# Performance work log

Measured on AMD Instinct MI355X. Metric: run time of the kernel, lower is better.

The kernel has to match this reference:

```python
import jax, jax.numpy as jnp
import numpy as np

STRIDE = 1
PADDING = 1
DILATION = 1

def setup_inputs() -> dict:
    key = jax.random.key(0)
    k1, k2, k3 = jax.random.split(key, 3)
    N, C_IN, H, W = 32, 384, 56, 56
    C_OUT, K = 384, 3
    x = jax.random.normal(k1, (N, C_IN, H, W), dtype=jnp.float32)
    w_dw = jax.random.normal(k2, (C_IN, 1, K, K), dtype=jnp.float32) * 0.1
    w_pw = jax.random.normal(k3, (C_OUT, C_IN, 1, 1), dtype=jnp.float32) * 0.05
    return {"x": x, "w_dw": w_dw, "w_pw": w_pw}

def reference(x, w_dw, w_pw):
    # Depthwise KxK conv: groups = C_IN (feature_group_count=C_IN)
    C_IN = x.shape[1]
    dw = jax.lax.conv_general_dilated(
        x, w_dw,
        window_strides=(STRIDE, STRIDE),
        padding=[(PADDING, PADDING), (PADDING, PADDING)],
        rhs_dilation=(DILATION, DILATION),
        dimension_numbers=("NCHW", "OIHW", "NCHW"),
        feature_group_count=C_IN,
    )  # [N, C_IN, H_out, W_out]
    # Pointwise 1x1 conv as a channel contraction
    w = w_pw[:, :, 0, 0]  # [C_OUT, C_IN]
    y = jnp.einsum("nchw,oc->nohw", dw, w)
    return y
```

## Files before the change

### kernel.cpp

```cpp
#include <hip/hip_runtime.h>
#include <hip/hip_bf16.h>
#include <stdint.h>

typedef float  f32x4  __attribute__((ext_vector_type(4)));
typedef short  bf16x8 __attribute__((ext_vector_type(8)));
typedef short  bf16x4 __attribute__((ext_vector_type(4)));

#define C_IN   384
#define C_OUT  384
#define Hdim   56
#define Wdim   56
#define HWsz   3136
#define KC     32
#define NCHUNK 12
#define NOSUB  24
#define BSTR   ((size_t)HWsz * KC)
#define RB     4
#define NRB    (Hdim / RB)
#define NBLKDW (NRB * NCHUNK * 32)
#define NPREP  ((C_OUT * C_IN) / 256)

__device__ __forceinline__ short f2bf(float f) {
    union { float f; uint32_t u; } v; v.f = f;
    uint32_t u = v.u + (0x7FFFu + ((v.u >> 16) & 1u));
    return (short)(u >> 16);
}

__device__ __forceinline__ void stage16(const short* g, const short* l) {
    __builtin_amdgcn_global_load_lds(
        (const __attribute__((address_space(1))) void*)g,
        (__attribute__((address_space(3))) void*)l, 16, 0, 0);
}

template<int N> __device__ __forceinline__ void wait_vmcnt() {
    if constexpr (N == 0)      asm volatile("s_waitcnt vmcnt(0)" ::: "memory");
    else if constexpr (N == 1) asm volatile("s_waitcnt vmcnt(1)" ::: "memory");
    else                       asm volatile("s_waitcnt vmcnt(2)" ::: "memory");
}
__device__ __forceinline__ void block_barrier() {
    asm volatile("" ::: "memory");
    __builtin_amdgcn_s_barrier();
    asm volatile("" ::: "memory");
}

__device__ __forceinline__ void prep_w_one(const float* __restrict__ wpw,
                                           short* __restrict__ apre, int idx) {
    int j    = idx & 7;
    int lane = (idx >> 3) & 63;
    int osub = (idx >> 9) % NOSUB;
    int cblk = idx / (NOSUB * 512);
    int o = osub * 16 + (lane & 15);
    int c = cblk * KC + (lane >> 4) * 8 + j;
    apre[idx] = f2bf(wpw[o * C_IN + c]);
}

__global__ void prep_w_kernel(const float* __restrict__ wpw, short* __restrict__ apre) {
    int idx = blockIdx.x * 256 + threadIdx.x;
    if (idx < C_OUT * C_IN) prep_w_one(wpw, apre, idx);
}

__global__ __launch_bounds__(256) void dw_kernel(
    const float* __restrict__ x, const float* __restrict__ wdw,
    const float* __restrict__ wpw, short* __restrict__ apre,
    short* __restrict__ dwws) {

    const int p = (int)blockIdx.x;
    if (p >= NBLKDW) {
        const int idx = (p - NBLKDW) * 256 + (int)threadIdx.x;
        if (idx < C_OUT * C_IN) prep_w_one(wpw, apre, idx);
        return;
    }

    const int l  = (p & 7) * (NBLKDW / 8) + (p >> 3);
    const int rb   = l % NRB;
    const int cblk = (l / NRB) % NCHUNK;
    const int n    = l / (NRB * NCHUNK);

    const int wave = (int)threadIdx.x >> 6;
    const int lane = (int)threadIdx.x & 63;
    const int c0u  = __builtin_amdgcn_readfirstlane(cblk * KC + wave * 8);
    const int h0   = rb * RB;

    const float* xb = x + ((size_t)n * C_IN + c0u) * HWsz;

    float v[8][RB + 2];
#pragma unroll
    for (int q = 0; q < 8; ++q)
#pragma unroll
        for (int d = 0; d < RB + 2; ++d) {
            const int hh = h0 + d - 1;
            const bool ok = (hh >= 0) && (hh < Hdim) && (lane < Wdim);
            v[q][d] = ok ? xb[(size_t)q * HWsz + hh * Wdim + lane] : 0.f;
        }

    const float* wp = wdw + c0u * 9;
    float wk[8][9];
#pragma unroll
    for (int q = 0; q < 8; ++q)
#pragma unroll
        for (int t = 0; t < 9; ++t) wk[q][t] = wp[q * 9 + t];

    bf16x8 pk[RB];
#pragma unroll
    for (int q = 0; q < 8; ++q) {
        float lf[RB + 2], rt[RB + 2];
#pragma unroll
        for (int d = 0; d < RB + 2; ++d) {
            float u = __shfl_up(v[q][d], 1);
            if (lane == 0) u = 0.f;
            lf[d] = u;
            rt[d] = __shfl_down(v[q][d], 1);
        }
#pragma unroll
        for (int r = 0; r < RB; ++r) {
            float a = 0.f;
#pragma unroll
            for (int d = 0; d < 3; ++d) {
                a = fmaf(wk[q][d * 3 + 0], lf[r + d], a);
                a = fmaf(wk[q][d * 3 + 1], v[q][r + d], a);
                a = fmaf(wk[q][d * 3 + 2], rt[r + d], a);
            }
            pk[r][q] = f2bf(a);
        }
    }

    if (lane < Wdim) {
#pragma unroll
        for (int r = 0; r < RB; ++r) {
            const size_t off = (((size_t)n * NCHUNK + cblk) * HWsz
                               + (h0 + r) * Wdim + lane) * KC + wave * 8;
            *reinterpret_cast<bf16x8*>(dwws + off) = pk[r];
        }
    }
}

__global__ __launch_bounds__(256, 3) void pw_kernel(
    const short* __restrict__ apre, const short* __restrict__ dwws,
    float* __restrict__ y) {

    __shared__ __align__(16) short Bt[4][64 * KC];

    const int pb   = blockIdx.x;
    const int n    = blockIdx.y;
    const int wave = (int)threadIdx.x >> 6;
    const int lane = (int)threadIdx.x & 63;
    const int col  = lane & 15;
    const int kb   = lane >> 4;

    f32x4 acc[6][4];
#pragma unroll
    for (int m = 0; m < 6; ++m)
#pragma unroll
        for (int p = 0; p < 4; ++p) acc[m][p] = (f32x4)0.f;

    const int pix_s = (wave << 4) + (lane >> 2);
    const int kbg   = (lane & 3) ^ ((lane >> 3) & 3);
    const short* gsrc0 = dwws + (size_t)n * NCHUNK * BSTR
                       + ((size_t)pb * 64 + pix_s) * KC + kbg * 8;
    const short* lbase = &Bt[0][0] + (wave << 9);

    int rd[4];
#pragma unroll
    for (int q = 0; q < 4; ++q) {
        const int pix = q * 16 + col;
        rd[q] = pix * KC + ((kb ^ ((pix >> 1) & 3)) << 3);
    }

#define STAGE(b, ch) stage16(gsrc0 + (size_t)(ch) * BSTR, lbase + (b) * (64 * KC))

    STAGE(0, 0);
    STAGE(1, 1);
    STAGE(2, 2);

#pragma unroll
    for (int ch = 0; ch < NCHUNK; ++ch) {
        if (ch <= NCHUNK - 3)      wait_vmcnt<2>();
        else if (ch == NCHUNK - 2) wait_vmcnt<1>();
        else                       wait_vmcnt<0>();
        block_barrier();

        bf16x8 af[6];
#pragma unroll
        for (int m = 0; m < 6; ++m)
            af[m] = *reinterpret_cast<const bf16x8*>(
                apre + (((ch * NOSUB + wave * 6 + m) * 64 + lane) << 3));

        if (ch + 3 < NCHUNK) STAGE((ch + 3) & 3, ch + 3);

        bf16x8 bfr[4];
#pragma unroll
        for (int q = 0; q < 4; ++q)
            bfr[q] = *reinterpret_cast<const bf16x8*>(&Bt[ch & 3][rd[q]]);

#pragma unroll
        for (int m = 0; m < 6; ++m)
#pragma unroll
            for (int q = 0; q < 4; ++q)
                acc[m][q] = __builtin_amdgcn_mfma_f32_16x16x32_bf16(
                    af[m], bfr[q], acc[m][q], 0, 0, 0);
    }
#undef STAGE

#pragma unroll
    for (int m = 0; m < 6; ++m) {
        const int o = wave * 96 + m * 16 + kb * 4;
        float* yo = y + ((size_t)(n * C_OUT + o)) * HWsz + pb * 64;
#pragma unroll
        for (int q = 0; q < 4; ++q) {
            const int pix = q * 16 + col;
#pragma unroll
            for (int r = 0; r < 4; ++r)
                __builtin_nontemporal_store(acc[m][q][r], yo + (size_t)r * HWsz + pix);
        }
    }
}

#define LDSS 40
__global__ __launch_bounds__(512) void fused_dwpw_kernel(
    const float* __restrict__ x, const float* __restrict__ wdw,
    const short* __restrict__ apre, float* __restrict__ y) {

    __shared__ __align__(16) short dw_lds[64 * LDSS];

    const int h    = blockIdx.x;
    const int n    = blockIdx.y;
    const int tid  = (int)threadIdx.x;
    const int wave = tid >> 6;
    const int lane = tid & 63;
    const int col  = lane & 15;
    const int kb   = lane >> 4;

    f32x4 acc[3][4];
#pragma unroll
    for (int m = 0; m < 3; ++m)
#pragma unroll
        for (int p = 0; p < 4; ++p) acc[m][p] = (f32x4)0.f;

    const float* xn = x + (size_t)n * C_IN * HWsz;

    for (int ch = 0; ch < NCHUNK; ++ch) {
        short dwv[4];
#pragma unroll
        for (int q = 0; q < 4; ++q) {
            const int c = ch * KC + wave * 4 + q;
            const float* xc = xn + (size_t)c * HWsz;
            const float* wkp = wdw + c * 9;
            float a0 = 0.f;
#pragma unroll
            for (int r = 0; r < 3; ++r) {
                const int hh = h + r - 1;
                float xv = 0.f;
                if (hh >= 0 && hh < Hdim && lane < Wdim) xv = xc[hh * Wdim + lane];
                float lf = __shfl_up(xv, 1);
                if (lane == 0) lf = 0.f;
                float rt = __shfl_down(xv, 1);
                a0 = fmaf(wkp[r * 3 + 0], lf, a0);
                a0 = fmaf(wkp[r * 3 + 1], xv, a0);
                a0 = fmaf(wkp[r * 3 + 2], rt, a0);
            }
            if (lane >= Wdim) a0 = 0.f;
            dwv[q] = f2bf(a0);
        }

        __syncthreads();
        {
            bf16x4 pk2; pk2[0] = dwv[0]; pk2[1] = dwv[1]; pk2[2] = dwv[2]; pk2[3] = dwv[3];
            *reinterpret_cast<bf16x4*>(&dw_lds[lane * LDSS + wave * 4]) = pk2;
        }
        __syncthreads();

        bf16x8 afr[3], bfr[4];
#pragma unroll
        for (int m = 0; m < 3; ++m)
            afr[m] = *reinterpret_cast<const bf16x8*>(
                apre + (((ch * NOSUB + wave * 3 + m) * 64 + lane) << 3));
#pragma unroll
        for (int p = 0; p < 4; ++p)
            bfr[p] = *reinterpret_cast<const bf16x8*>(
                &dw_lds[(p * 16 + col) * LDSS + kb * 8]);
#pragma unroll
        for (int m = 0; m < 3; ++m)
#pragma unroll
            for (int p = 0; p < 4; ++p)
                acc[m][p] = __builtin_amdgcn_mfma_f32_16x16x32_bf16(
                    afr[m], bfr[p], acc[m][p], 0, 0, 0);
    }

#pragma unroll
    for (int p = 0; p < 4; ++p) {
        const int pix = p * 16 + col;
        if (pix >= Wdim) continue;
#pragma unroll
        for (int m = 0; m < 3; ++m) {
            const int o0 = wave * 48 + m * 16 + kb * 4;
            float* yp = y + ((size_t)(n * C_OUT + o0)) * HWsz + h * Wdim + pix;
#pragma unroll
            for (int r = 0; r < 4; ++r) yp[(size_t)r * HWsz] = acc[m][p][r];
        }
    }
}

extern "C" void kernel_launch(void* const* d_in, const int* in_sizes, int n_in,
                              void* d_out, int out_size, void* d_ws, size_t ws_size,
                              hipStream_t stream) {
    const float* x   = (const float*)d_in[0];
    const float* wdw = (const float*)d_in[1];
    const float* wpw = (const float*)d_in[2];
    float* y = (float*)d_out;

    short* apre = (short*)d_ws;
    const size_t DW_OFF   = 512 * 1024;
    const size_t DW_BYTES = (size_t)32 * HWsz * C_IN * 2;

    if (ws_size >= DW_OFF + DW_BYTES) {
        short* dwws = (short*)((char*)d_ws + DW_OFF);
        hipLaunchKernelGGL(dw_kernel, dim3(NBLKDW + NPREP), dim3(256),
                           0, stream, x, wdw, wpw, apre, dwws);
        hipLaunchKernelGGL(pw_kernel, dim3(HWsz / 64, 32), dim3(256),
                           0, stream, apre, dwws, y);
    } else {
        hipLaunchKernelGGL(prep_w_kernel, dim3((C_OUT * C_IN + 255) / 256), dim3(256),
                           0, stream, wpw, apre);
        hipLaunchKernelGGL(fused_dwpw_kernel, dim3(Hdim, 32), dim3(512),
                           0, stream, x, wdw, apre, y);
    }
}
```

Measured before the change: 106.9 us.

## Restructure depthwise stencil with packed bf16 shuffles and slab layout for intermediate

The depthwise stage now computes the three column partial sums per row first and exchanges only the left and right partials between lanes, packed as bf16 pairs with v_cvt_pk_bf16_f32. This cuts the shuffle count compared with shuffling every input row. The intermediate buffer changes from pixel-major 32-channel interleave to per-wave 8-channel slabs, and the pointwise kernel's global-to-LDS staging and read addresses get a new XOR swizzle to match. Rounding the side partials to bf16 before summing adds a small accuracy loss.

Result: faster. 96.44 us (median of 3 runs) (-9.8%).

```diff
diff --git a/kernel.cpp b/kernel.cpp
--- a/kernel.cpp
+++ b/kernel.cpp
@@ -14,6 +14,7 @@
 #define KC     32
 #define NCHUNK 12
 #define NOSUB  24
+#define SLAB   ((size_t)HWsz * 8)
 #define BSTR   ((size_t)HWsz * KC)
 #define RB     4
 #define NRB    (Hdim / RB)
@@ -24,6 +25,12 @@
     union { float f; uint32_t u; } v; v.f = f;
     uint32_t u = v.u + (0x7FFFu + ((v.u >> 16) & 1u));
     return (short)(u >> 16);
+}
+
+__device__ __forceinline__ uint32_t cvtpk_bf16(float lo, float hi) {
+    uint32_t r;
+    asm("v_cvt_pk_bf16_f32 %0, %1, %2" : "=v"(r) : "v"(lo), "v"(hi));
+    return r;
 }
 
 __device__ __forceinline__ void stage16(const short* g, const short* l) {
@@ -102,35 +109,39 @@
 
     bf16x8 pk[RB];
 #pragma unroll
-    for (int q = 0; q < 8; ++q) {
-        float lf[RB + 2], rt[RB + 2];
-#pragma unroll
-        for (int d = 0; d < RB + 2; ++d) {
-            float u = __shfl_up(v[q][d], 1);
-            if (lane == 0) u = 0.f;
-            lf[d] = u;
-            rt[d] = __shfl_down(v[q][d], 1);
-        }
+    for (int qq = 0; qq < 8; qq += 2) {
 #pragma unroll
         for (int r = 0; r < RB; ++r) {
-            float a = 0.f;
+            float tA[3], tB[3];
 #pragma unroll
             for (int d = 0; d < 3; ++d) {
-                a = fmaf(wk[q][d * 3 + 0], lf[r + d], a);
-                a = fmaf(wk[q][d * 3 + 1], v[q][r + d], a);
-                a = fmaf(wk[q][d * 3 + 2], rt[r + d], a);
+                tA[d] = wk[qq][d] * v[qq][r];
+                tA[d] = fmaf(wk[qq][3 + d], v[qq][r + 1], tA[d]);
+                tA[d] = fmaf(wk[qq][6 + d], v[qq][r + 2], tA[d]);
+                tB[d] = wk[qq + 1][d] * v[qq + 1][r];
+                tB[d] = fmaf(wk[qq + 1][3 + d], v[qq + 1][r + 1], tB[d]);
+                tB[d] = fmaf(wk[qq + 1][6 + d], v[qq + 1][r + 2], tB[d]);
             }
-            pk[r][q] = f2bf(a);
+            uint32_t p0 = cvtpk_bf16(tA[0], tB[0]);
+            uint32_t p2 = cvtpk_bf16(tA[2], tB[2]);
+            uint32_t l0 = __shfl_up(p0, 1);
+            if (lane == 0) l0 = 0u;
+            uint32_t r2 = __shfl_down(p2, 1);
+            const float lfA = __uint_as_float(l0 << 16);
+            const float lfB = __uint_as_float(l0 & 0xFFFF0000u);
+            const float rtA = __uint_as_float(r2 << 16);
+            const float rtB = __uint_as_float(r2 & 0xFFFF0000u);
+            pk[r][qq]     = f2bf(tA[1] + lfA + rtA);
+            pk[r][qq + 1] = f2bf(tB[1] + lfB + rtB);
         }
     }
 
     if (lane < Wdim) {
-#pragma unroll
-        for (int r = 0; r < RB; ++r) {
-            const size_t off = (((size_t)n * NCHUNK + cblk) * HWsz
-                               + (h0 + r) * Wdim + lane) * KC + wave * 8;
-            *reinterpret_cast<bf16x8*>(dwws + off) = pk[r];
-        }
+        short* sb = dwws + (((size_t)n * NCHUNK + cblk) * 4 + wave) * SLAB;
+#pragma unroll
+        for (int r = 0; r < RB; ++r)
+            *reinterpret_cast<bf16x8*>(sb + ((size_t)(h0 + r) * Wdim + lane) * 8)
+                = pk[r];
     }
 }
 
@@ -151,19 +162,19 @@
 #pragma unroll
     for (int m = 0; m < 6; ++m)
 #pragma unroll
-        for (int p = 0; p < 4; ++p) acc[m][p] = (f32x4)0.f;
-
-    const int pix_s = (wave << 4) + (lane >> 2);
-    const int kbg   = (lane & 3) ^ ((lane >> 3) & 3);
-    const short* gsrc0 = dwws + (size_t)n * NCHUNK * BSTR
-                       + ((size_t)pb * 64 + pix_s) * KC + kbg * 8;
+        for (int q = 0; q < 4; ++q) acc[m][q] = (f32x4)0.f;
+
+    const int plog = (lane & ~7) | ((lane ^ (lane >> 3) ^ (wave << 1)) & 7);
+    const short* gsrc0 = dwws + (size_t)n * NCHUNK * BSTR + (size_t)wave * SLAB
+                       + ((size_t)pb * 64 + plog) * 8;
     const short* lbase = &Bt[0][0] + (wave << 9);
 
     int rd[4];
 #pragma unroll
     for (int q = 0; q < 4; ++q) {
         const int pix = q * 16 + col;
-        rd[q] = pix * KC + ((kb ^ ((pix >> 1) & 3)) << 3);
+        const int ppx = (pix & ~7) | ((pix ^ (pix >> 3) ^ (kb << 1)) & 7);
+        rd[q] = (kb * 64 + ppx) * 8;
     }
 
 #define STAGE(b, ch) stage16(gsrc0 + (size_t)(ch) * BSTR, lbase + (b) * (64 * KC))
```
